# Performance work log

Hardware: AMD Instinct MI355X
Metric: run time of the kernel (lower is better)

The kernel has to match this reference:

```python
import jax, jax.numpy as jnp
import numpy as np

B, D_IN, D_HID, D_OUT = 16384, 512, 512, 512
E, K = 8, 2
VQ_COEFF, LB_COEFF = 0.05, 0.01
LOG100 = float(np.log(100.0))
LOG2 = float(np.log(2.0))


def _normalize(v):
    # torch F.normalize(dim=1): x / max(||x||, 1e-12)
    n = jnp.linalg.norm(v, axis=-1, keepdims=True)
    return v / jnp.maximum(n, 1e-12)


def _cv_squared(v):
    # torch .var() is unbiased (ddof=1)
    return jnp.var(v, ddof=1) / (jnp.mean(v) ** 2 + 1e-10)


def _rbm_layer(x, rm, W, b, ca, temp):
    # x: [B, d_in], rm: [E, d_in], W: [E, d_out, d_in], b: [E, d_out]
    rm_n = jax.lax.stop_gradient(_normalize(rm))          # .detach() in source
    nx = _normalize(x)
    dists = nx @ rm_n.T                                    # [B, E]
    top_v, top_i = jax.lax.top_k(dists, K)                 # [B, K]
    tv = jax.nn.softmax(top_v, axis=-1)                    # softmax over top-k
    bsz = dists.shape[0]
    attn = jnp.zeros_like(dists).at[jnp.arange(bsz)[:, None], top_i].set(tv)
    # const_attention is frozen (requires_grad=False)
    inp_att = jnp.exp(jnp.minimum(jax.lax.stop_gradient(ca), LOG100))  # [E]
    # dense gather-compute-scatter: expert e output for every token, masked by attn
    eo = jnp.einsum('bi,eoi->beo', x, W) * inp_att[None, :, None] + b[None, :, :]
    out = jnp.einsum('be,beo->bo', jax.lax.stop_gradient(attn), eo)    # att.detach()
    out = out * jnp.exp(jnp.minimum(temp, LOG100))
    # aux losses (eval mode: no EMA memory update)
    vq = -(nx[:, None, :] * rm_n[top_i]).sum(-1)           # [B, K]
    vq_loss = (tv * vq).sum(-1).mean()
    lb = _cv_squared(attn.sum(0))
    aux = VQ_COEFF * vq_loss + LB_COEFF * lb               # sim_coeff = 0
    return out, aux


def setup_inputs() -> dict:
    key = jax.random.key(0)
    ks = jax.random.split(key, 8)
    x = jax.random.normal(ks[0], (B, D_IN), dtype=jnp.float32)
    rm0 = _normalize(jax.random.normal(ks[1], (E, D_IN), dtype=jnp.float32))
    W0 = jax.random.normal(ks[2], (E, D_HID, D_IN), dtype=jnp.float32) / np.sqrt(D_IN)
    b0 = jnp.zeros((E, D_HID), dtype=jnp.float32)
    rm1 = _normalize(jax.random.normal(ks[3], (E, D_HID), dtype=jnp.float32))
    W1 = jax.random.normal(ks[4], (E, D_OUT, D_HID), dtype=jnp.float32) / np.sqrt(D_HID)
    b1 = jnp.zeros((E, D_OUT), dtype=jnp.float32)
    temp0 = jnp.full((1,), LOG2, dtype=jnp.float32)
    temp1 = jnp.full((1,), LOG2, dtype=jnp.float32)
    ca0 = jnp.zeros((E,), dtype=jnp.float32)
    ca1 = jnp.zeros((E,), dtype=jnp.float32)
    return {"x": x, "rm0": rm0, "W0": W0, "b0": b0, "temp0": temp0, "ca0": ca0,
            "rm1": rm1, "W1": W1, "b1": b1, "temp1": temp1, "ca1": ca1}


def reference(x, rm0, W0, b0, temp0, ca0, rm1, W1, b1, temp1, ca1):
    h0, a0 = _rbm_layer(x, rm0, W0, b0, ca0, temp0)
    h_emb = h0                      # embedding tapped after layer 0 (pre-activation)
    h = jax.nn.relu(h0)             # norm_type=None -> no norm
    h1, a1 = _rbm_layer(h, rm1, W1, b1, ca1, temp1)
    return (h_emb, h1, a0 + a1)
```

## Files before the change

### kernel.cpp

```cpp
#include <hip/hip_runtime.h>
#include <cmath>
#include <cstdint>

#define NTOK   16384
#define NEXP   8
#define DM     512
#define LOG100 4.605170185988092f

typedef _Float16 half8  __attribute__((ext_vector_type(8)));
typedef float    floatx4 __attribute__((ext_vector_type(4)));

#define MFMA_F16(a, b, c) __builtin_amdgcn_mfma_f32_16x16x32_f16((a), (b), (c), 0, 0, 0)

__device__ __forceinline__ void gl_lds16(const void* g, void* l) {
    __builtin_amdgcn_global_load_lds(
        (const __attribute__((address_space(1))) void*)g,
        (__attribute__((address_space(3))) void*)l, 16, 0, 0);
}

__device__ __forceinline__ void atomAddF(float* p, float v) {
#if __has_builtin(__builtin_amdgcn_global_atomic_fadd_f32)
    __builtin_amdgcn_global_atomic_fadd_f32((__attribute__((address_space(1))) float*)p, v);
#else
    atomicAdd(p, v);
#endif
}


__global__ __launch_bounds__(256) void pack_w_kernel(
    const float* __restrict__ W0, const float* __restrict__ W1,
    half8* __restrict__ w0pk, half8* __restrict__ w1pk,
    const float* __restrict__ rm0, const float* __restrict__ rm1,
    const float* __restrict__ ca0, const float* __restrict__ ca1,
    const float* __restrict__ temp0, const float* __restrict__ temp1,
    float* __restrict__ ctrl, float* __restrict__ rmn)
{
    if (blockIdx.x == 3072) {
        int tid = threadIdx.x, lane = tid & 63, w = tid >> 6;
        if (tid < 32) ((int*)ctrl)[tid] = 0;
        if (tid >= 32 && tid < 48) ctrl[tid] = 0.f;
        if (tid == 48 || tid == 49) ctrl[tid] = 0.f;
        if (tid == 50) ctrl[50] = expf(fminf(temp0[0], LOG100));
        if (tid == 51) ctrl[51] = expf(fminf(temp1[0], LOG100));
        if (tid >= 52 && tid < 68) {
            int i = tid - 52;
            ctrl[tid] = expf(fminf(i < 8 ? ca0[i] : ca1[i - 8], LOG100));
        }
        for (int r = w; r < 16; r += 4) {
            const float* src = (r < 8) ? (rm0 + r * DM) : (rm1 + (r - 8) * DM);
            float v[8]; float ss = 0.f;
            #pragma unroll
            for (int j = 0; j < 8; ++j) { v[j] = src[lane + 64 * j]; ss += v[j] * v[j]; }
            #pragma unroll
            for (int off = 32; off > 0; off >>= 1) ss += __shfl_xor(ss, off);
            float inv = 1.f / fmaxf(sqrtf(ss), 1e-12f);
            float* dst = rmn + r * DM;
            #pragma unroll
            for (int j = 0; j < 8; ++j) dst[lane + 64 * j] = v[j] * inv;
        }
        return;
    }
    int i = blockIdx.x * 256 + threadIdx.x;
    if (i < 512 * 1024) {
        int l = i & 63, j = (i >> 6) & 15, kb = (i >> 10) & 15, nt = (i >> 14) & 3, e = i >> 16;
        int s = l >> 3, p = l & 7, c = p ^ s;
        int n = nt * 128 + j * 8 + s;
        int k = kb * 32 + (c & 3) * 8;
        const float* src = W0 + ((size_t)e * DM + n) * DM + k;
        half8 v;
        #pragma unroll
        for (int t = 0; t < 8; ++t) {
            float f = src[t];
            _Float16 h = (_Float16)f;
            v[t] = (c < 4) ? h : (_Float16)(f - (float)h);
        }
        w0pk[i] = v;
    } else {
        int m = i - 512 * 1024;
        int l = m & 63, j = (m >> 6) & 15, kb = (m >> 10) & 7, nt = (m >> 13) & 3, e = m >> 15;
        int s = l >> 3, p = l & 7, c = p ^ s;
        int n = nt * 128 + j * 8 + s;
        int k = kb * 64 + c * 8;
        const float* src = W1 + ((size_t)e * DM + n) * DM + k;
        half8 v;
        #pragma unroll
        for (int t = 0; t < 8; ++t) v[t] = (_Float16)src[t];
        w1pk[m] = v;
    }
}

__global__ __launch_bounds__(256) void route_kernel(
    const float* __restrict__ src,
    const float* __restrict__ rmn,
    int relu_in, int split,
    _Float16* __restrict__ dst,
    unsigned char* __restrict__ key,
    float2* __restrict__ wts,
    float2* __restrict__ bs,
    float* __restrict__ zrow)
{
    __shared__ float rmLds[NEXP * DM];
    int tid = threadIdx.x;
    for (int i = tid; i < NEXP * DM; i += 256) rmLds[i] = rmn[i];
    __syncthreads();
    int lane = tid & 63, w = tid >> 6;
    int token = blockIdx.x * 4 + w;

    {
        float4 z4 = {0.f, 0.f, 0.f, 0.f};
        float4* zp = (float4*)(zrow + (size_t)token * DM);
        zp[lane] = z4;
        zp[lane + 64] = z4;
    }

    const float* row = src + (size_t)token * DM;
    float x[8]; float ss = 0.f;
    #pragma unroll
    for (int j = 0; j < 8; ++j) {
        float v = row[lane + 64 * j];
        if (relu_in) v = fmaxf(v, 0.f);
        x[j] = v; ss += v * v;
    }
    if (split) {
        #pragma unroll
        for (int j = 0; j < 8; ++j) {
            int k = lane + 64 * j;
            size_t base = (size_t)token * 1024 + (size_t)((k >> 5) << 6) + (k & 31);
            _Float16 h = (_Float16)x[j];
            dst[base] = h;
            dst[base + 32] = (_Float16)(x[j] - (float)h);
        }
    } else {
        #pragma unroll
        for (int j = 0; j < 8; ++j)
            dst[(size_t)token * DM + lane + 64 * j] = (_Float16)x[j];
    }
    float d[8];
    #pragma unroll
    for (int e = 0; e < 8; ++e) {
        float a = 0.f;
        #pragma unroll
        for (int j = 0; j < 8; ++j) a += x[j] * rmLds[e * DM + lane + 64 * j];
        d[e] = a;
    }
    #pragma unroll
    for (int off = 32; off > 0; off >>= 1) {
        ss += __shfl_xor(ss, off);
        #pragma unroll
        for (int e = 0; e < 8; ++e) d[e] += __shfl_xor(d[e], off);
    }
    float inv = 1.f / fmaxf(sqrtf(ss), 1e-12f);
    float best = -1e30f, second = -1e30f; int be = 0, se = 0;
    #pragma unroll
    for (int e = 0; e < 8; ++e) {
        float de = d[e] * inv;
        if (de > best)        { second = best; se = be; best = de; be = e; }
        else if (de > second) { second = de; se = e; }
    }
    float z = expf(second - best);
    float w0 = 1.f / (1.f + z), w1 = z / (1.f + z);
    if (lane == 0) {
        key[token] = (unsigned char)be;
        key[NTOK + token] = (unsigned char)se;
        wts[token] = make_float2(w0, w1);
        bs[token] = make_float2(best, second);
    }
}

__global__ __launch_bounds__(256) void compact_kernel(
    const unsigned char* __restrict__ key,
    const float2* __restrict__ wts,
    const float2* __restrict__ bs,
    int* __restrict__ cnt,
    unsigned short* __restrict__ bkt,
    float* __restrict__ imp,
    float* __restrict__ vq_acc)
{
    int slot = blockIdx.x >> 3, e = blockIdx.x & 7;
    int chunk = blockIdx.y;
    const unsigned char* k = key + slot * NTOK;
    unsigned short* ob = bkt + (size_t)(slot * 8 + e) * NTOK;
    int tid = threadIdx.x, lane = tid & 63, w = tid >> 6;
    float wsum = 0.f, vqs = 0.f;
    for (int c = 0; c < 8; ++c) {
        int tok = chunk * 2048 + c * 256 + tid;
        bool m = (k[tok] == (unsigned char)e);
        unsigned long long mask = __ballot(m);
        int wcount = __popcll(mask);
        int wbase = 0;
        if (lane == 0 && wcount) wbase = atomicAdd(&cnt[slot * 8 + e], wcount);
        wbase = __shfl(wbase, 0);
        if (m) {
            int pre = __popcll(mask & ((1ull << lane) - 1ull));
            ob[wbase + pre] = (unsigned short)tok;
            float2 wp = wts[tok]; float2 b2 = bs[tok];
            float wv = slot ? wp.y : wp.x;
            wsum += wv;
            vqs  += wv * (slot ? b2.y : b2.x);
        }
    }
    #pragma unroll
    for (int off = 32; off > 0; off >>= 1) {
        wsum += __shfl_xor(wsum, off);
        vqs  += __shfl_xor(vqs, off);
    }
    __shared__ float rw[4], rv[4];
    if (lane == 0) { rw[w] = wsum; rv[w] = vqs; }
    __syncthreads();
    if (tid == 0) {
        atomicAdd(&imp[e], rw[0] + rw[1] + rw[2] + rw[3]);
        atomicAdd(vq_acc, -(rv[0] + rv[1] + rv[2] + rv[3]));
    }
}

template <bool SPLIT>
__global__ __launch_bounds__(64) void gemm_kernel(
    const _Float16* __restrict__ A,
    const _Float16* __restrict__ Wpk,
    const float* __restrict__ bias,
    const float* __restrict__ iav,
    const float* __restrict__ tscp,
    const int* __restrict__ cnt16,
    const unsigned short* __restrict__ bkt,
    const float2* __restrict__ wts,
    float* __restrict__ outp)
{
    __shared__ __align__(16) _Float16 ldsB[2 * 4096];
    __shared__ int tokLds[64];

    int bx = blockIdx.x;
    int xcd = bx & 7, sIdx = bx >> 3;
    int t = xcd * 66 + (sIdx >> 3), nt64 = sIdx & 7;
    int b = -1, m0 = 0, M = 0, acc0 = 0;
    #pragma unroll
    for (int bb = 0; bb < 16; ++bb) {
        int Me = cnt16[bb];
        int ne = (Me + 63) >> 6;
        if (t >= acc0 && t < acc0 + ne) { b = bb; m0 = (t - acc0) << 6; M = Me; }
        acc0 += ne;
    }
    if (b < 0) return;
    int slot = b >> 3, e = b & 7;
    int n0 = nt64 << 6;
    int valid = min(64, M - m0);
    int lane = threadIdx.x;
    int q = lane >> 4, l15 = lane & 15;

    tokLds[lane] = bkt[(size_t)b * NTOK + m0 + min(lane, valid - 1)];

    constexpr int KIT = SPLIT ? 16 : 8;
    constexpr int AS  = SPLIT ? 1024 : 512;

    const _Float16* Ab[4];
    #pragma unroll
    for (int mi = 0; mi < 4; ++mi)
        Ab[mi] = A + (size_t)tokLds[mi * 16 + l15] * AS + q * 8;

    const _Float16* wtile = Wpk + ((size_t)(e * 4 + (nt64 >> 1)) * KIT) * 8192
                                + (size_t)(nt64 & 1) * 8 * 512;

    floatx4 accu[4][4];
    #pragma unroll
    for (int mi = 0; mi < 4; ++mi)
        #pragma unroll
        for (int ni = 0; ni < 4; ++ni) accu[mi][ni] = (floatx4){0.f, 0.f, 0.f, 0.f};

    half8 ahR[2][4], alR[2][4];

    #pragma unroll
    for (int mi = 0; mi < 4; ++mi) {
        ahR[0][mi] = *(const half8*)(Ab[mi]);
        alR[0][mi] = *(const half8*)(Ab[mi] + 32);
    }
    #pragma unroll
    for (int jj = 0; jj < 8; ++jj)
        gl_lds16(wtile + jj * 512 + lane * 8, (void*)(ldsB + jj * 512));

    #pragma unroll
    for (int kb = 0; kb < KIT; ++kb) {
        int cu = kb & 1, nx = cu ^ 1;
        if (kb + 1 < KIT) {
            #pragma unroll
            for (int mi = 0; mi < 4; ++mi) {
                ahR[nx][mi] = *(const half8*)(Ab[mi] + (kb + 1) * 64);
                alR[nx][mi] = *(const half8*)(Ab[mi] + (kb + 1) * 64 + 32);
            }
            const _Float16* wb = wtile + (size_t)(kb + 1) * 8192;
            _Float16* dB = ldsB + nx * 4096;
            #pragma unroll
            for (int jj = 0; jj < 8; ++jj)
                gl_lds16(wb + jj * 512 + lane * 8, (void*)(dB + jj * 512));
            asm volatile("s_waitcnt vmcnt(16)" ::: "memory");
        } else {
            asm volatile("s_waitcnt vmcnt(0)" ::: "memory");
        }
        __builtin_amdgcn_sched_barrier(0);
        {
            const _Float16* bB = ldsB + cu * 4096;
            #pragma unroll
            for (int ni = 0; ni < 4; ++ni) {
                int r = ni * 16 + l15;
                int ph = q ^ (r & 7), pl = (q + 4) ^ (r & 7);
                half8 bh = *(const half8*)(bB + r * 64 + ph * 8);
                half8 bl = *(const half8*)(bB + r * 64 + pl * 8);
                if constexpr (SPLIT) {
                    #pragma unroll
                    for (int mi = 0; mi < 4; ++mi) accu[mi][ni] = MFMA_F16(ahR[cu][mi], bh, accu[mi][ni]);
                    #pragma unroll
                    for (int mi = 0; mi < 4; ++mi) accu[mi][ni] = MFMA_F16(ahR[cu][mi], bl, accu[mi][ni]);
                    #pragma unroll
                    for (int mi = 0; mi < 4; ++mi) accu[mi][ni] = MFMA_F16(alR[cu][mi], bh, accu[mi][ni]);
                } else {
                    #pragma unroll
                    for (int mi = 0; mi < 4; ++mi) accu[mi][ni] = MFMA_F16(ahR[cu][mi], bh, accu[mi][ni]);
                    #pragma unroll
                    for (int mi = 0; mi < 4; ++mi) accu[mi][ni] = MFMA_F16(alR[cu][mi], bl, accu[mi][ni]);
                }
            }
        }
    }

    float tsc = *tscp, iae = iav[e];
    float bv[4];
    #pragma unroll
    for (int ni = 0; ni < 4; ++ni) bv[ni] = bias[e * DM + n0 + ni * 16 + l15];
    #pragma unroll
    for (int mi = 0; mi < 4; ++mi) {
        int liBase = mi * 16 + q * 4;
        #pragma unroll
        for (int reg = 0; reg < 4; ++reg) {
            int li = liBase + reg;
            if (li < valid) {
                int tok = tokLds[li];
                float2 wp = wts[tok];
                float wgt = slot ? wp.y : wp.x;
                float sg = tsc * wgt * iae, sb = tsc * wgt;
                float* orow = outp + (size_t)tok * DM + n0;
                #pragma unroll
                for (int ni = 0; ni < 4; ++ni) {
                    float v = accu[mi][ni][reg] * sg + bv[ni] * sb;
                    int c = ni * 16 + l15;
                    atomAddF(&orow[c], v);
                }
            }
        }
    }
}

__global__ void finalize_kernel(const float* __restrict__ ctrl, float* __restrict__ outp)
{
    if (threadIdx.x == 0) {
        float aux = 0.f;
        for (int l = 0; l < 2; ++l) {
            float vq = ctrl[48 + l] / (float)NTOK;
            float mean = 0.f;
            for (int e = 0; e < 8; ++e) mean += ctrl[32 + l * 8 + e];
            mean *= 0.125f;
            float s = 0.f;
            for (int e = 0; e < 8; ++e) {
                float d = ctrl[32 + l * 8 + e] - mean;
                s += d * d;
            }
            float var = s / 7.f;
            float lb = var / (mean * mean + 1e-10f);
            aux += 0.05f * vq + 0.01f * lb;
        }
        *outp = aux;
    }
}

extern "C" void kernel_launch(void* const* d_in, const int* in_sizes, int n_in,
                              void* d_out, int out_size, void* d_ws, size_t ws_size,
                              hipStream_t stream) {
    const float* x     = (const float*)d_in[0];
    const float* rm0   = (const float*)d_in[1];
    const float* W0    = (const float*)d_in[2];
    const float* b0    = (const float*)d_in[3];
    const float* temp0 = (const float*)d_in[4];
    const float* ca0   = (const float*)d_in[5];
    const float* rm1   = (const float*)d_in[6];
    const float* W1    = (const float*)d_in[7];
    const float* b1    = (const float*)d_in[8];
    const float* temp1 = (const float*)d_in[9];
    const float* ca1   = (const float*)d_in[10];
    float* out = (float*)d_out;

    char* ws = (char*)d_ws;
    float* ctrl = (float*)ws;
    int*   cnt  = (int*)ctrl;
    float* imp  = ctrl + 32;
    float* vq   = ctrl + 48;
    float* tsc  = ctrl + 50;
    float* ia   = ctrl + 52;
    float* rmn  = ctrl + 128;
    float2*        wts = (float2*)(ws + (size_t)64  * 1024);
    float2*        bs  = (float2*)(ws + (size_t)384 * 1024);
    unsigned char* key = (unsigned char*)(ws + (size_t)704 * 1024);

    char* big = ws + (1 << 20);
    half8*          w0pk8 = (half8*)(big);
    half8*          w1pk8 = (half8*)(big + (size_t)8  * 1024 * 1024);
    const _Float16* w0pk  = (const _Float16*)w0pk8;
    const _Float16* w1pk  = (const _Float16*)w1pk8;
    _Float16*       h16   = (_Float16*)(big + (size_t)12 * 1024 * 1024);
    unsigned short* bkt   = (unsigned short*)(big + (size_t)28 * 1024 * 1024);

    _Float16* xpk = (_Float16*)(out + (size_t)NTOK * DM);

    const int GEMM_GRID = 528 * 8;

    pack_w_kernel<<<3073, 256, 0, stream>>>(W0, W1, w0pk8, w1pk8,
        rm0, rm1, ca0, ca1, temp0, temp1, ctrl, rmn);

    route_kernel<<<4096, 256, 0, stream>>>(x, rmn, 0, 1, xpk, key, wts, bs, out);
    compact_kernel<<<dim3(16, 8), 256, 0, stream>>>(key, wts, bs, cnt, bkt, imp, vq);
    gemm_kernel<true><<<GEMM_GRID, 64, 0, stream>>>(xpk, w0pk, b0, ia, tsc,
        cnt, bkt, wts, out);

    route_kernel<<<4096, 256, 0, stream>>>(out, rmn + 4096, 1, 0, h16,
        key + 2 * NTOK, wts + NTOK, bs + NTOK, out + (size_t)NTOK * DM);
    compact_kernel<<<dim3(16, 8), 256, 0, stream>>>(key + 2 * NTOK, wts + NTOK, bs + NTOK,
        cnt + 16, bkt + 16 * NTOK, imp + 8, vq + 1);
    gemm_kernel<false><<<GEMM_GRID, 64, 0, stream>>>(h16, w1pk, b1, ia + 8, tsc + 1,
        cnt + 16, bkt + 16 * NTOK, wts + NTOK, out + (size_t)NTOK * DM);

    finalize_kernel<<<1, 64, 0, stream>>>(ctrl, out + (size_t)2 * NTOK * DM);
}
```

Before: 451.3 us.

## Replace atomic scatter-add with per-slot partial buffers and explicit sum

The GEMM epilogue now writes each top-k slot's contribution with plain stores into one of two partial buffers (output or a workspace buffer), instead of doing float atomic adds into a zeroed output. Layer 0's partials are summed inside the second route kernel, which also writes h_emb back. Layer 1's partials are summed by a new elementwise kernel. This removes atomic contention and the zeroing pass, at the cost of an extra 32MB partial buffer of traffic and one more kernel launch.

```diff
diff --git a/kernel.cpp b/kernel.cpp
--- a/kernel.cpp
+++ b/kernel.cpp
@@ -16,14 +16,6 @@
     __builtin_amdgcn_global_load_lds(
         (const __attribute__((address_space(1))) void*)g,
         (__attribute__((address_space(3))) void*)l, 16, 0, 0);
-}
-
-__device__ __forceinline__ void atomAddF(float* p, float v) {
-#if __has_builtin(__builtin_amdgcn_global_atomic_fadd_f32)
-    __builtin_amdgcn_global_atomic_fadd_f32((__attribute__((address_space(1))) float*)p, v);
-#else
-    atomicAdd(p, v);
-#endif
 }
 
 
@@ -91,13 +83,14 @@
 
 __global__ __launch_bounds__(256) void route_kernel(
     const float* __restrict__ src,
+    const float* __restrict__ src2,
     const float* __restrict__ rmn,
     int relu_in, int split,
     _Float16* __restrict__ dst,
+    float* __restrict__ sumOut,
     unsigned char* __restrict__ key,
     float2* __restrict__ wts,
-    float2* __restrict__ bs,
-    float* __restrict__ zrow)
+    float2* __restrict__ bs)
 {
     __shared__ float rmLds[NEXP * DM];
     int tid = threadIdx.x;
@@ -106,18 +99,16 @@
     int lane = tid & 63, w = tid >> 6;
     int token = blockIdx.x * 4 + w;
 
-    {
-        float4 z4 = {0.f, 0.f, 0.f, 0.f};
-        float4* zp = (float4*)(zrow + (size_t)token * DM);
-        zp[lane] = z4;
-        zp[lane + 64] = z4;
-    }
-
-    const float* row = src + (size_t)token * DM;
+    const float* row  = src + (size_t)token * DM;
+    const float* row2 = src2 ? (src2 + (size_t)token * DM) : nullptr;
+    float* so = sumOut ? (sumOut + (size_t)token * DM) : nullptr;
     float x[8]; float ss = 0.f;
     #pragma unroll
     for (int j = 0; j < 8; ++j) {
-        float v = row[lane + 64 * j];
+        int k = lane + 64 * j;
+        float v = row[k];
+        if (row2) v += row2[k];
+        if (so) so[k] = v;
         if (relu_in) v = fmaxf(v, 0.f);
         x[j] = v; ss += v * v;
     }
@@ -223,7 +214,8 @@
     const int* __restrict__ cnt16,
     const unsigned short* __restrict__ bkt,
     const float2* __restrict__ wts,
-    float* __restrict__ outp)
+    float* __restrict__ outP0,
+    float* __restrict__ outP1)
 {
     __shared__ __align__(16) _Float16 ldsB[2 * 4096];
     __shared__ int tokLds[64];
@@ -321,6 +313,7 @@
     }
 
     float tsc = *tscp, iae = iav[e];
+    float* outP = slot ? outP1 : outP0;
     float bv[4];
     #pragma unroll
     for (int ni = 0; ni < 4; ++ni) bv[ni] = bias[e * DM + n0 + ni * 16 + l15];
@@ -335,16 +328,23 @@
                 float2 wp = wts[tok];
                 float wgt = slot ? wp.y : wp.x;
                 float sg = tsc * wgt * iae, sb = tsc * wgt;
-                float* orow = outp + (size_t)tok * DM + n0;
+                float* orow = outP + (size_t)tok * DM + n0;
                 #pragma unroll
                 for (int ni = 0; ni < 4; ++ni) {
-                    float v = accu[mi][ni][reg] * sg + bv[ni] * sb;
                     int c = ni * 16 + l15;
-                    atomAddF(&orow[c], v);
+                    orow[c] = accu[mi][ni][reg] * sg + bv[ni] * sb;
                 }
             }
         }
     }
+}
+
+__global__ __launch_bounds__(256) void sum_kernel(
+    const float4* __restrict__ a, const float4* __restrict__ b, float4* __restrict__ o)
+{
+    int i = blockIdx.x * 256 + threadIdx.x;
+    float4 va = a[i], vb = b[i];
+    o[i] = make_float4(va.x + vb.x, va.y + vb.y, va.z + vb.z, va.w + vb.w);
 }
 
 __global__ void finalize_kernel(const float* __restrict__ ctrl, float* __restrict__ outp)
@@ -404,25 +404,30 @@
     const _Float16* w1pk  = (const _Float16*)w1pk8;
     _Float16*       h16   = (_Float16*)(big + (size_t)12 * 1024 * 1024);
     unsigned short* bkt   = (unsigned short*)(big + (size_t)28 * 1024 * 1024);
-
+    float*          Pbuf  = (float*)(big + (size_t)30 * 1024 * 1024);
+
+    float*    P0  = out;
     _Float16* xpk = (_Float16*)(out + (size_t)NTOK * DM);
+    float*    Q0  = out + (size_t)NTOK * DM;
 
     const int GEMM_GRID = 528 * 8;
 
     pack_w_kernel<<<3073, 256, 0, stream>>>(W0, W1, w0pk8, w1pk8,
         rm0, rm1, ca0, ca1, temp0, temp1, ctrl, rmn);
 
-    route_kernel<<<4096, 256, 0, stream>>>(x, rmn, 0, 1, xpk, key, wts, bs, out);
+    route_kernel<<<4096, 256, 0, stream>>>(x, (const float*)nullptr, rmn, 0, 1,
+        xpk, (float*)nullptr, key, wts, bs);
     compact_kernel<<<dim3(16, 8), 256, 0, stream>>>(key, wts, bs, cnt, bkt, imp, vq);
     gemm_kernel<true><<<GEMM_GRID, 64, 0, stream>>>(xpk, w0pk, b0, ia, tsc,
-        cnt, bkt, wts, out);
-
-    route_kernel<<<4096, 256, 0, stream>>>(out, rmn + 4096, 1, 0, h16,
-        key + 2 * NTOK, wts + NTOK, bs + NTOK, out + (size_t)NTOK * DM);
+        cnt, bkt, wts, P0, Pbuf);
+
+    route_kernel<<<4096, 256, 0, stream>>>(P0, Pbuf, rmn + 4096, 1, 0,
+        h16, P0, key + 2 * NTOK, wts + NTOK, bs + NTOK);
     compact_kernel<<<dim3(16, 8), 256, 0, stream>>>(key + 2 * NTOK, wts + NTOK, bs + NTOK,
         cnt + 16, bkt + 16 * NTOK, imp + 8, vq + 1);
     gemm_kernel<false><<<GEMM_GRID, 64, 0, stream>>>(h16, w1pk, b1, ia + 8, tsc + 1,
-        cnt + 16, bkt + 16 * NTOK, wts + NTOK, out + (size_t)NTOK * DM);
+        cnt + 16, bkt + 16 * NTOK, wts + NTOK, Q0, Pbuf);
+    sum_kernel<<<8192, 256, 0, stream>>>((const float4*)Q0, (const float4*)Pbuf, (float4*)Q0);
 
     finalize_kernel<<<1, 64, 0, stream>>>(ctrl, out + (size_t)2 * NTOK * DM);
 }
```

Result: faster. 430.2 us (-4.7%).
